# Optimization experiments

Hardware: AMD Instinct MI355X
Metric: run time of the kernel (lower is better)

Reference implementation:

```python
import jax, jax.numpy as jnp
import numpy as np

N = 200000
IN_CH = 128
HIDDEN = [512, 512, 256]
NUM_TYPES = 10


def hetero_linear(x, types, W, b):
    # y[n] = x[n] @ W[types[n]] + b[types[n]]
    # Loop over the small fixed set of types (grouped GEMM as masked dense GEMMs).
    out = jnp.zeros((x.shape[0], W.shape[2]), dtype=x.dtype)
    for t in range(W.shape[0]):
        yt = x @ W[t] + b[t]
        out = out + jnp.where((types == t)[:, None], yt, jnp.zeros((), x.dtype))
    return out


def setup_inputs() -> dict:
    key = jax.random.key(0)
    ks = jax.random.split(key, 8)
    dims = [IN_CH] + HIDDEN
    inp = {
        "x": jax.random.normal(ks[0], (N, IN_CH), dtype=jnp.float32),
        "atom_types": jax.random.randint(ks[1], (N,), 0, NUM_TYPES, dtype=jnp.int32),
    }
    for i in range(3):
        fan_in = dims[i]
        scale = 1.0 / np.sqrt(fan_in)
        inp[f"W{i}"] = jax.random.normal(ks[2 + 2 * i], (NUM_TYPES, dims[i], dims[i + 1]), dtype=jnp.float32) * scale
        inp[f"b{i}"] = jax.random.normal(ks[3 + 2 * i], (NUM_TYPES, dims[i + 1]), dtype=jnp.float32) * scale
    return inp


def reference(x, atom_types, W0, b0, W1, b1, W2, b2):
    h = jax.nn.relu(hetero_linear(x, atom_types, W0, b0))
    h = jax.nn.relu(hetero_linear(h, atom_types, W1, b1))
    return hetero_linear(h, atom_types, W2, b2)
```

## Files before the change

### kernel.cpp

```cpp
#include <hip/hip_runtime.h>
#include <stdint.h>

typedef float  f32x4  __attribute__((ext_vector_type(4)));
typedef short  bf16x8 __attribute__((ext_vector_type(8)));

#define TYPES 10
#define D_IN  128
#define D_H1  512
#define D_H2  512
#define D_OUT 256

__device__ __forceinline__ unsigned short f2bf(float f) {
  union { float f; unsigned u; } v; v.f = f;
  unsigned u = v.u;
  return (unsigned short)((u + 0x7FFFu + ((u >> 16) & 1u)) >> 16);
}

__device__ __forceinline__ void async16(void* lds, const void* g) {
  __builtin_amdgcn_global_load_lds(
      (const __attribute__((address_space(1))) void*)g,
      (__attribute__((address_space(3))) void*)lds, 16, 0, 0);
}

__global__ void k_init(int* meta) {
  if (threadIdx.x < 48) meta[threadIdx.x] = 0;
}

__global__ void k_hist(const int* __restrict__ types, int n, int* __restrict__ meta) {
  __shared__ int lc[TYPES];
  if (threadIdx.x < TYPES) lc[threadIdx.x] = 0;
  __syncthreads();
  int i = blockIdx.x * 256 + threadIdx.x;
  if (i < n) atomicAdd(&lc[types[i]], 1);
  __syncthreads();
  if (threadIdx.x < TYPES && lc[threadIdx.x]) atomicAdd(&meta[threadIdx.x], lc[threadIdx.x]);
}

__global__ void k_scan(int* meta) {
  if (threadIdx.x == 0) {
    int off = 0;
    for (int t = 0; t < TYPES; ++t) {
      meta[16 + t] = off;
      off += ((meta[t] + 255) >> 8) << 8;
    }
    meta[26] = off;
  }
}

__global__ void k_scatter(const int* __restrict__ types, int n,
                          int* __restrict__ meta, int* __restrict__ perm) {
  __shared__ int lc[TYPES], lbase[TYPES];
  if (threadIdx.x < TYPES) lc[threadIdx.x] = 0;
  __syncthreads();
  int i = blockIdx.x * 256 + threadIdx.x;
  int t = 0, loc = 0;
  bool ok = i < n;
  if (ok) { t = types[i]; loc = atomicAdd(&lc[t], 1); }
  __syncthreads();
  if (threadIdx.x < TYPES) {
    int c = lc[threadIdx.x];
    lbase[threadIdx.x] = c ? atomicAdd(&meta[32 + threadIdx.x], c) : 0;
  }
  __syncthreads();
  if (ok) perm[meta[16 + t] + lbase[t] + loc] = i;
}

__global__ void k_gather(const float* __restrict__ x, const int* __restrict__ perm,
                         const int* __restrict__ meta, unsigned short* __restrict__ xs) {
  int p = blockIdx.x * 8 + (threadIdx.x >> 5);
  if (p >= meta[26]) return;
  int t = 0;
  while (p >= meta[17 + t]) t++;
  int e = (threadIdx.x & 31) * 4;
  unsigned short o0, o1, o2, o3;
  if (p - meta[16 + t] < meta[t]) {
    const float4 v = *(const float4*)(x + (size_t)perm[p] * D_IN + e);
    o0 = f2bf(v.x); o1 = f2bf(v.y); o2 = f2bf(v.z); o3 = f2bf(v.w);
  } else {
    o0 = o1 = o2 = o3 = 0;
  }
  *(ushort4*)(xs + (size_t)p * D_IN + e) = make_ushort4(o0, o1, o2, o3);
}

__global__ void k_wtrans(const float* __restrict__ W, unsigned short* __restrict__ Wt,
                         int K, int NOUT) {
  int t = blockIdx.y;
  int ntn = NOUT >> 6;
  int kb = blockIdx.x / ntn, nb = blockIdx.x % ntn;
  __shared__ unsigned short tile[64][65];
  const float* src = W + (size_t)t * K * NOUT + (size_t)(kb * 64) * NOUT + nb * 64;
  int c = threadIdx.x & 63;
  int r0 = threadIdx.x >> 6;
  #pragma unroll
  for (int i = 0; i < 16; ++i) {
    int r = r0 * 16 + i;
    tile[r][c] = f2bf(src[(size_t)r * NOUT + c]);
  }
  __syncthreads();
  unsigned short* dst = Wt + (size_t)t * NOUT * K + (size_t)(nb * 64) * K + kb * 64;
  #pragma unroll
  for (int i = 0; i < 16; ++i) {
    int nn = r0 * 16 + i;
    dst[(size_t)nn * K + c] = tile[c][nn];
  }
}

template <int K, int NOUT, bool RELU, bool FINAL>
__launch_bounds__(512, 2)
__global__ void k_gemm(const unsigned short* __restrict__ A,
                       const unsigned short* __restrict__ Wt,
                       const float* __restrict__ bias,
                       unsigned short* __restrict__ H,
                       float* __restrict__ OUT,
                       const int* __restrict__ meta,
                       const int* __restrict__ perm) {
  constexpr int nKT = K / 64;
  __shared__ char lds[131072];

  int NXB = gridDim.x;
  int nwg = NXB * (int)gridDim.y;
  int raw = blockIdx.x + blockIdx.y * NXB;
  int q = nwg >> 3, rr = nwg & 7;
  int xcd = raw & 7, idx = raw >> 3;
  int swz = (xcd < rr ? xcd * (q + 1) : rr * (q + 1) + (xcd - rr) * q) + idx;
  int bx = swz % NXB, by = swz / NXB;

  int row0 = by * 256;
  if (row0 >= meta[26]) return;
  int t = 0;
  while (row0 >= meta[17 + t]) t++;
  int seg = meta[16 + t], cnt = meta[t];
  int tid = threadIdx.x, lane = tid & 63, wid = tid >> 6;
  int wr = (wid >> 2) * 128, wc = (wid & 3) * 64;
  int col0 = bx * 256;
  const char* Ag = (const char*)(A + (size_t)row0 * K);
  const char* Bg = (const char*)(Wt + ((size_t)t * NOUT + col0) * K);

  int gsrc = ((tid & 7) ^ ((tid >> 3) & 7)) * 16;
  const char* aS = Ag + (size_t)(tid >> 3) * (2 * K) + gsrc;
  const char* bS = Bg + (size_t)(((tid >> 3) & 31) + ((tid >> 3) >> 5) * 64) * (2 * K) + gsrc;

  auto stage = [&](int kt, int sub) {
    if (kt >= nKT) return;
    int h = sub & 1, du = kt & 1;
    char* dst = lds + ((sub < 2) ? 0 : 65536) + (du * 2 + h) * 16384 + wid * 1024;
    const char* src = (sub < 2 ? aS + (size_t)(h * 64) * (2 * K)
                               : bS + (size_t)(h * 32) * (2 * K)) + (size_t)kt * 128;
    async16(dst,        src);
    async16(dst + 8192, src + (size_t)128 * (2 * K));
  };

  f32x4 acc[8][4] = {};
  int rA = lane & 15, qoff = (lane >> 4) * 16, xr = (lane & 7) << 4;
  int lrA = (wid >> 2) * 64;
  int clB = (wid & 3) * 32;

  stage(0, 0); stage(0, 1); stage(0, 2); stage(0, 3); stage(1, 0);
  asm volatile("s_waitcnt vmcnt(2)" ::: "memory");
  __builtin_amdgcn_s_barrier();

  for (int g = 0; g < nKT; ++g) {
    int d = g & 1;
    const char* Ad = lds + d * 32768;
    const char* Bd = lds + 65536 + d * 32768;
    bf16x8 a[4][2], b[2][2];
    #pragma unroll
    for (int rel = 0; rel < 4; ++rel) {
      constexpr int MH[4] = {0, 0, 1, 1};
      constexpr int NH[4] = {0, 1, 1, 0};
      const int mh = MH[rel], nh = NH[rel];
      if (rel == 0 || rel == 2) {
        const char* Au = Ad + mh * 16384;
        #pragma unroll
        for (int m = 0; m < 4; ++m) {
          int lr = lrA + m * 16 + rA;
          #pragma unroll
          for (int kk = 0; kk < 2; ++kk)
            a[m][kk] = *(const bf16x8*)(Au + ((lr * 128 + kk * 64 + qoff) ^ xr));
        }
      }
      if (rel != 2) {
        const char* Bu = Bd + nh * 16384;
        #pragma unroll
        for (int nn = 0; nn < 2; ++nn) {
          int cl = clB + nn * 16 + rA;
          #pragma unroll
          for (int kk = 0; kk < 2; ++kk)
            b[nn][kk] = *(const bf16x8*)(Bu + ((cl * 128 + kk * 64 + qoff) ^ xr));
        }
      }
      if      (rel == 0) stage(g + 1, 1);
      else if (rel == 1) stage(g + 1, 2);
      else if (rel == 2) stage(g + 1, 3);
      else               stage(g + 2, 0);
      __builtin_amdgcn_s_barrier();
      asm volatile("s_waitcnt lgkmcnt(0)" ::: "memory");
      __builtin_amdgcn_sched_barrier(0);
      __builtin_amdgcn_s_setprio(1);
      #pragma unroll
      for (int kk = 0; kk < 2; ++kk)
        #pragma unroll
        for (int m = 0; m < 4; ++m)
          #pragma unroll
          for (int nn = 0; nn < 2; ++nn)
            acc[mh * 4 + m][nh * 2 + nn] = __builtin_amdgcn_mfma_f32_16x16x32_bf16(
                a[m][kk], b[nn][kk], acc[mh * 4 + m][nh * 2 + nn], 0, 0, 0);
      __builtin_amdgcn_s_setprio(0);
      if (rel == 3 && g + 1 < nKT) {
        if (g + 2 < nKT) asm volatile("s_waitcnt vmcnt(2)" ::: "memory");
        else             asm volatile("s_waitcnt vmcnt(0)" ::: "memory");
      }
      __builtin_amdgcn_s_barrier();
    }
  }

  int cA = lane & 15, rE = (lane >> 4) * 4;
  float bv[4];
  #pragma unroll
  for (int ni = 0; ni < 4; ++ni) bv[ni] = bias[t * NOUT + col0 + wc + ni * 16 + cA];
  char* cb = (char*)lds;

  if (!FINAL) {
    #pragma unroll
    for (int mi = 0; mi < 8; ++mi)
      #pragma unroll
      for (int e = 0; e < 4; ++e) {
        int row = wr + mi * 16 + rE + e;
        int sw = (row & 7) << 4;
        #pragma unroll
        for (int ni = 0; ni < 4; ++ni) {
          float v = acc[mi][ni][e] + bv[ni];
          if (RELU) v = fmaxf(v, 0.f);
          int col = wc + ni * 16 + cA;
          *(unsigned short*)(cb + ((row * 512 + col * 2) ^ sw)) = f2bf(v);
        }
      }
    __builtin_amdgcn_s_barrier();
    #pragma unroll 4
    for (int r = 0; r < 16; ++r) {
      int row = wid * 32 + r * 2 + (lane >> 5);
      int addr = row * 512 + ((((lane & 31) * 16)) ^ ((row & 7) << 4));
      bf16x8 v = *(const bf16x8*)(cb + addr);
      *(bf16x8*)(H + (size_t)(row0 + row) * NOUT + col0 + (lane & 31) * 8) = v;
    }
  } else {
    int myhalf = (wid & 3) >> 1;
    #pragma unroll
    for (int p = 0; p < 2; ++p) {
      if (myhalf == p) {
        int colh = wc & 127;
        #pragma unroll
        for (int mi = 0; mi < 8; ++mi)
          #pragma unroll
          for (int e = 0; e < 4; ++e) {
            int row = wr + mi * 16 + rE + e;
            int sw = (row & 7) << 4;
            #pragma unroll
            for (int ni = 0; ni < 4; ++ni) {
              float v = acc[mi][ni][e] + bv[ni];
              if (RELU) v = fmaxf(v, 0.f);
              int col = colh + ni * 16 + cA;
              *(float*)(cb + ((row * 512 + col * 4) ^ sw)) = v;
            }
          }
      }
      __builtin_amdgcn_s_barrier();
      #pragma unroll 4
      for (int r = 0; r < 16; ++r) {
        int row = wid * 32 + r * 2 + (lane >> 5);
        int gr = row0 + row;
        int addr = row * 512 + ((((lane & 31) * 16)) ^ ((row & 7) << 4));
        float4 v = *(const float4*)(cb + addr);
        if (gr - seg < cnt) {
          int pr = perm[gr];
          *(float4*)(OUT + (size_t)pr * NOUT + p * (NOUT / 2) + (lane & 31) * 4) = v;
        }
      }
      if (p == 0) __builtin_amdgcn_s_barrier();
    }
  }
}

extern "C" void kernel_launch(void* const* d_in, const int* in_sizes, int n_in,
                              void* d_out, int out_size, void* d_ws, size_t ws_size,
                              hipStream_t stream) {
  const float* x     = (const float*)d_in[0];
  const int*   types = (const int*)d_in[1];
  const float* W0    = (const float*)d_in[2];
  const float* b0    = (const float*)d_in[3];
  const float* W1    = (const float*)d_in[4];
  const float* b1    = (const float*)d_in[5];
  const float* W2    = (const float*)d_in[6];
  const float* b2    = (const float*)d_in[7];
  float* out = (float*)d_out;
  int n = in_sizes[1];
  int RB = (n + 255) / 256 + TYPES;
  size_t NPAD = (size_t)RB * 256;

  char* ws = (char*)d_ws;
  int* meta = (int*)ws;
  int* perm = (int*)(ws + 1024);
  size_t off = 1024 + NPAD * 4;
  off = (off + 255) & ~(size_t)255;
  unsigned short* wt0 = (unsigned short*)(ws + off); off += (size_t)TYPES * D_H1 * D_IN * 2;
  unsigned short* wt1 = (unsigned short*)(ws + off); off += (size_t)TYPES * D_H2 * D_H1 * 2;
  unsigned short* wt2 = (unsigned short*)(ws + off); off += (size_t)TYPES * D_OUT * D_H2 * 2;
  off = (off + 255) & ~(size_t)255;
  unsigned short* B1 = (unsigned short*)(ws + off); off += NPAD * 512 * 2;
  unsigned short* B2 = (unsigned short*)(ws + off); off += NPAD * 512 * 2;

  int hb = (n + 255) / 256;
  k_init<<<1, 64, 0, stream>>>(meta);
  k_hist<<<hb, 256, 0, stream>>>(types, n, meta);
  k_scan<<<1, 64, 0, stream>>>(meta);
  k_scatter<<<hb, 256, 0, stream>>>(types, n, meta, perm);
  k_gather<<<RB * 32, 256, 0, stream>>>(x, perm, meta, B1);
  k_wtrans<<<dim3((D_IN / 64) * (D_H1 / 64), TYPES), 256, 0, stream>>>(W0, wt0, D_IN, D_H1);
  k_wtrans<<<dim3((D_H1 / 64) * (D_H2 / 64), TYPES), 256, 0, stream>>>(W1, wt1, D_H1, D_H2);
  k_wtrans<<<dim3((D_H2 / 64) * (D_OUT / 64), TYPES), 256, 0, stream>>>(W2, wt2, D_H2, D_OUT);

  k_gemm<D_IN, D_H1, true,  false><<<dim3(D_H1 / 256, RB), 512, 0, stream>>>(B1, wt0, b0, B2, nullptr, meta, perm);
  k_gemm<D_H1, D_H2, true,  false><<<dim3(D_H2 / 256, RB), 512, 0, stream>>>(B2, wt1, b1, B1, nullptr, meta, perm);
  k_gemm<D_H2, D_OUT, false, true ><<<dim3(D_OUT / 256, RB), 512, 0, stream>>>(B1, wt2, b2, nullptr, out, meta, perm);
}
```

Baseline: 435.6 us.

## Restage GEMM B-fragment loads with double registers and merge weight transposes into one launch

The GEMM main loop now keeps both halves of the B fragments in separate registers (b0/b1). Both halves are loaded early in the first two sub-phases, and the async LDS staging is issued earlier with adjusted vmcnt wait depths, so more global loads stay in flight. The three per-layer weight transpose kernels are fused into a single launch that dispatches on block index, cutting launch overhead. The B double-buffering raises register pressure, and the new wait counts must match the issued load counts exactly or correctness suffers.

```diff
diff --git a/kernel.cpp b/kernel.cpp
--- a/kernel.cpp
+++ b/kernel.cpp
@@ -82,11 +82,17 @@
   *(ushort4*)(xs + (size_t)p * D_IN + e) = make_ushort4(o0, o1, o2, o3);
 }
 
-__global__ void k_wtrans(const float* __restrict__ W, unsigned short* __restrict__ Wt,
-                         int K, int NOUT) {
-  int t = blockIdx.y;
+__global__ void k_wtrans_all(const float* __restrict__ W0a, const float* __restrict__ W1a,
+                             const float* __restrict__ W2a,
+                             unsigned short* __restrict__ wt0, unsigned short* __restrict__ wt1,
+                             unsigned short* __restrict__ wt2) {
+  int b = blockIdx.x;
+  const float* W; unsigned short* Wt; int K, NOUT, t, local;
+  if (b < 160)      { W = W0a; Wt = wt0; K = 128; NOUT = 512; t = b / 16; local = b % 16; }
+  else if (b < 800) { b -= 160; W = W1a; Wt = wt1; K = 512; NOUT = 512; t = b / 64; local = b % 64; }
+  else              { b -= 800; W = W2a; Wt = wt2; K = 512; NOUT = 256; t = b / 32; local = b % 32; }
   int ntn = NOUT >> 6;
-  int kb = blockIdx.x / ntn, nb = blockIdx.x % ntn;
+  int kb = local / ntn, nb = local % ntn;
   __shared__ unsigned short tile[64][65];
   const float* src = W + (size_t)t * K * NOUT + (size_t)(kb * 64) * NOUT + nb * 64;
   int c = threadIdx.x & 63;
@@ -156,16 +162,17 @@
   int clB = (wid & 3) * 32;
 
   stage(0, 0); stage(0, 1); stage(0, 2); stage(0, 3); stage(1, 0);
-  asm volatile("s_waitcnt vmcnt(2)" ::: "memory");
+  asm volatile("s_waitcnt vmcnt(4)" ::: "memory");
   __builtin_amdgcn_s_barrier();
 
   for (int g = 0; g < nKT; ++g) {
     int d = g & 1;
     const char* Ad = lds + d * 32768;
     const char* Bd = lds + 65536 + d * 32768;
-    bf16x8 a[4][2], b[2][2];
+    bf16x8 a[4][2], b0[2][2], b1[2][2];
     #pragma unroll
     for (int rel = 0; rel < 4; ++rel) {
+      __builtin_amdgcn_sched_barrier(0);
       constexpr int MH[4] = {0, 0, 1, 1};
       constexpr int NH[4] = {0, 1, 1, 0};
       const int mh = MH[rel], nh = NH[rel];
@@ -179,20 +186,29 @@
             a[m][kk] = *(const bf16x8*)(Au + ((lr * 128 + kk * 64 + qoff) ^ xr));
         }
       }
-      if (rel != 2) {
-        const char* Bu = Bd + nh * 16384;
+      if (rel == 0) {
+        const char* Bu = Bd;
         #pragma unroll
         for (int nn = 0; nn < 2; ++nn) {
           int cl = clB + nn * 16 + rA;
           #pragma unroll
           for (int kk = 0; kk < 2; ++kk)
-            b[nn][kk] = *(const bf16x8*)(Bu + ((cl * 128 + kk * 64 + qoff) ^ xr));
-        }
-      }
-      if      (rel == 0) stage(g + 1, 1);
-      else if (rel == 1) stage(g + 1, 2);
-      else if (rel == 2) stage(g + 1, 3);
-      else               stage(g + 2, 0);
+            b0[nn][kk] = *(const bf16x8*)(Bu + ((cl * 128 + kk * 64 + qoff) ^ xr));
+        }
+      }
+      if (rel == 1) {
+        const char* Bu = Bd + 16384;
+        #pragma unroll
+        for (int nn = 0; nn < 2; ++nn) {
+          int cl = clB + nn * 16 + rA;
+          #pragma unroll
+          for (int kk = 0; kk < 2; ++kk)
+            b1[nn][kk] = *(const bf16x8*)(Bu + ((cl * 128 + kk * 64 + qoff) ^ xr));
+        }
+      }
+      if      (rel == 0) { stage(g + 1, 1); stage(g + 1, 2); }
+      else if (rel == 1) stage(g + 1, 3);
+      else if (rel == 3) stage(g + 2, 0);
       __builtin_amdgcn_s_barrier();
       asm volatile("s_waitcnt lgkmcnt(0)" ::: "memory");
       __builtin_amdgcn_sched_barrier(0);
@@ -202,13 +218,18 @@
         #pragma unroll
         for (int m = 0; m < 4; ++m)
           #pragma unroll
-          for (int nn = 0; nn < 2; ++nn)
+          for (int nn = 0; nn < 2; ++nn) {
+            const bf16x8 bop = nh ? b1[nn][kk] : b0[nn][kk];
             acc[mh * 4 + m][nh * 2 + nn] = __builtin_amdgcn_mfma_f32_16x16x32_bf16(
-                a[m][kk], b[nn][kk], acc[mh * 4 + m][nh * 2 + nn], 0, 0, 0);
+                a[m][kk], bop, acc[mh * 4 + m][nh * 2 + nn], 0, 0, 0);
+          }
       __builtin_amdgcn_s_setprio(0);
-      if (rel == 3 && g + 1 < nKT) {
-        if (g + 2 < nKT) asm volatile("s_waitcnt vmcnt(2)" ::: "memory");
+      if (rel == 0) {
+        if (g + 1 < nKT) asm volatile("s_waitcnt vmcnt(6)" ::: "memory");
         else             asm volatile("s_waitcnt vmcnt(0)" ::: "memory");
+      } else if (rel == 3 && g + 1 < nKT) {
+        if (g + 2 < nKT) asm volatile("s_waitcnt vmcnt(4)" ::: "memory");
+        else             asm volatile("s_waitcnt vmcnt(2)" ::: "memory");
       }
       __builtin_amdgcn_s_barrier();
     }
@@ -315,9 +336,7 @@
   k_scan<<<1, 64, 0, stream>>>(meta);
   k_scatter<<<hb, 256, 0, stream>>>(types, n, meta, perm);
   k_gather<<<RB * 32, 256, 0, stream>>>(x, perm, meta, B1);
-  k_wtrans<<<dim3((D_IN / 64) * (D_H1 / 64), TYPES), 256, 0, stream>>>(W0, wt0, D_IN, D_H1);
-  k_wtrans<<<dim3((D_H1 / 64) * (D_H2 / 64), TYPES), 256, 0, stream>>>(W1, wt1, D_H1, D_H2);
-  k_wtrans<<<dim3((D_H2 / 64) * (D_OUT / 64), TYPES), 256, 0, stream>>>(W2, wt2, D_H2, D_OUT);
+  k_wtrans_all<<<1120, 256, 0, stream>>>(W0, W1, W2, wt0, wt1, wt2);
 
   k_gemm<D_IN, D_H1, true,  false><<<dim3(D_H1 / 256, RB), 512, 0, stream>>>(B1, wt0, b0, B2, nullptr, meta, perm);
   k_gemm<D_H1, D_H2, true,  false><<<dim3(D_H2 / 256, RB), 512, 0, stream>>>(B2, wt1, b1, B1, nullptr, meta, perm);
```

Result: faster. 423.9 us (-2.7%).
